# Optimization experiments

Hardware: AMD Instinct MI355X
Metric: run time of the kernel (lower is better)

The kernel has to match this reference:

```python
import jax, jax.numpy as jnp
import numpy as np

D_MODEL = 1024
N_HEADS = 16
D_HEAD = D_MODEL // N_HEADS
B, T = 2, 2048


def setup_inputs() -> dict:
    key = jax.random.key(0)
    ks = jax.random.split(key, 8)
    s = 1.0 / np.sqrt(D_MODEL)
    return {
        "x": jax.random.normal(ks[0], (B, T, D_MODEL), dtype=jnp.float32),
        "ln_g": jnp.ones((D_MODEL,), jnp.float32),
        "ln_b": jnp.zeros((D_MODEL,), jnp.float32),
        "w_qkv": jax.random.normal(ks[1], (D_MODEL, 3 * D_MODEL), jnp.float32) * s,
        "b_qkv": jnp.zeros((3 * D_MODEL,), jnp.float32),
        "w_gate": jax.random.normal(ks[2], (D_MODEL, D_MODEL), jnp.float32) * s,
        "b_gate": jnp.zeros((D_MODEL,), jnp.float32),
        "w_proj": jax.random.normal(ks[3], (D_MODEL, D_MODEL), jnp.float32) * s,
        "b_proj": jnp.zeros((D_MODEL,), jnp.float32),
    }


def reference(x, ln_g, ln_b, w_qkv, b_qkv, w_gate, b_gate, w_proj, b_proj):
    Bb, Tt, Dd = x.shape
    H, dh = N_HEADS, D_HEAD

    # LayerNorm (eps=1e-5, torch default)
    mu = jnp.mean(x, axis=-1, keepdims=True)
    var = jnp.mean((x - mu) ** 2, axis=-1, keepdims=True)
    x_norm = (x - mu) / jnp.sqrt(var + 1e-5) * ln_g + ln_b

    qkv = x_norm @ w_qkv + b_qkv
    q, k, v = jnp.split(qkv, 3, axis=-1)

    # concept gate on the RAW input x (not x_norm), normalized by its mean
    gate_sig = jax.nn.sigmoid(x @ w_gate + b_gate)
    gate_norm = gate_sig / (jnp.mean(gate_sig, axis=-1, keepdims=True) + 1e-5)
    q = q * gate_norm
    k = k * gate_norm

    # [B,T,D] -> [B,H,T,dh]
    def to_heads(t):
        return t.reshape(Bb, Tt, H, dh).transpose(0, 2, 1, 3)

    q, k, v = to_heads(q), to_heads(k), to_heads(v)

    q = jax.nn.elu(q) + 1.0
    k = jax.nn.elu(k) + 1.0

    # materialized outer-product cumsum (faithful to source formulation)
    kv = jnp.einsum("bhtd,bhtm->bhtdm", k, v)          # [B,H,T,dh,dh]
    kv_cumsum = jnp.cumsum(kv, axis=2)
    out_num = jnp.einsum("bhtd,bhtdm->bhtm", q, kv_cumsum)
    k_cumsum = jnp.cumsum(k, axis=2)
    out_den = jnp.einsum("bhtd,bhtd->bht", q, k_cumsum)[..., None] + 1e-5
    out = out_num / out_den                              # [B,H,T,dh]

    out = out.transpose(0, 2, 1, 3).reshape(Bb, Tt, Dd)
    return out @ w_proj + b_proj
```

## Files before the change

kernel.cpp:

```cpp
#include <hip/hip_runtime.h>
#include <math.h>

constexpr int D      = 1024;
constexpr int H      = 16;
constexpr int DH     = 64;
constexpr int Bb     = 2;
constexpr int T      = 2048;
constexpr int BT     = Bb * T;
constexpr int CHUNK  = 64;
constexpr int NC     = T / CHUNK;
constexpr int LS     = 72;

typedef __attribute__((ext_vector_type(8))) short bf16x8;
typedef __attribute__((ext_vector_type(4))) float f32x4;

#define GLOAD_LDS16(gp, lp) \
    __builtin_amdgcn_global_load_lds((const __attribute__((address_space(1))) void*)(gp), \
                                     (__attribute__((address_space(3))) void*)(lp), 16, 0, 0)

__device__ __forceinline__ short to_bf16(float f) {
    unsigned u = __float_as_uint(f);
    unsigned r = (u + 0x7fffu + ((u >> 16) & 1u)) >> 16;
    return (short)r;
}
__device__ __forceinline__ float bf2f(short s) {
    return __uint_as_float(((unsigned)(unsigned short)s) << 16);
}

__device__ __forceinline__ float block_sum_256(float v, float* sbuf) {
    #pragma unroll
    for (int off = 32; off > 0; off >>= 1) v += __shfl_down(v, off, 64);
    int lane = threadIdx.x & 63;
    int wid  = threadIdx.x >> 6;
    if (lane == 0) sbuf[wid] = v;
    __syncthreads();
    float r = (threadIdx.x < 4) ? sbuf[threadIdx.x] : 0.0f;
    r += __shfl_down(r, 2, 64);
    r += __shfl_down(r, 1, 64);
    if (threadIdx.x == 0) sbuf[0] = r;
    __syncthreads();
    float outv = sbuf[0];
    __syncthreads();
    return outv;
}

__device__ __forceinline__ float elu1(float x) {
    return x > 0.0f ? x + 1.0f : expf(x);
}

__global__ __launch_bounds__(256) void ln_kernel(const float* __restrict__ x,
                                                 const float* __restrict__ g,
                                                 const float* __restrict__ b,
                                                 short* __restrict__ ynb,
                                                 short* __restrict__ xb) {
    __shared__ float sbuf[4];
    int row = blockIdx.x;
    const float* xr = x + (size_t)row * D;
    int c = threadIdx.x * 4;
    float4 xv = *(const float4*)(xr + c);
    float mu = block_sum_256(xv.x + xv.y + xv.z + xv.w, sbuf) * (1.0f / D);
    float d0 = xv.x - mu, d1 = xv.y - mu, d2 = xv.z - mu, d3 = xv.w - mu;
    float var = block_sum_256(d0*d0 + d1*d1 + d2*d2 + d3*d3, sbuf) * (1.0f / D);
    float rstd = rsqrtf(var + 1e-5f);
    float4 gv = *(const float4*)(g + c);
    float4 bv = *(const float4*)(b + c);
    short4 o, xo;
    o.x = to_bf16(d0 * rstd * gv.x + bv.x);
    o.y = to_bf16(d1 * rstd * gv.y + bv.y);
    o.z = to_bf16(d2 * rstd * gv.z + bv.z);
    o.w = to_bf16(d3 * rstd * gv.w + bv.w);
    xo.x = to_bf16(xv.x); xo.y = to_bf16(xv.y);
    xo.z = to_bf16(xv.z); xo.w = to_bf16(xv.w);
    *(short4*)(ynb + (size_t)row * D + c) = o;
    *(short4*)(xb  + (size_t)row * D + c) = xo;
}

__global__ __launch_bounds__(256) void transpose_all_kernel(const float* __restrict__ wq,
                                                            const float* __restrict__ wg,
                                                            const float* __restrict__ wp,
                                                            short* __restrict__ wTcomb,
                                                            short* __restrict__ wTp) {
    __shared__ short tile[32][33];
    int bid = blockIdx.x;
    const float* W; short* Wt; int N; int t;
    if (bid < 3072)      { W = wq; Wt = wTcomb;                        N = 3072; t = bid; }
    else if (bid < 4096) { W = wg; Wt = wTcomb + (size_t)3072 * 1024;  N = 1024; t = bid - 3072; }
    else                 { W = wp; Wt = wTp;                           N = 1024; t = bid - 4096; }
    int ntiles = N >> 5;
    int nb = (t % ntiles) * 32, kb = (t / ntiles) * 32;
    int tx = threadIdx.x & 31, ty = threadIdx.x >> 5;
    #pragma unroll
    for (int i = 0; i < 4; ++i) {
        int k = kb + ty + i * 8;
        tile[ty + i * 8][tx] = to_bf16(W[(size_t)k * N + nb + tx]);
    }
    __syncthreads();
    #pragma unroll
    for (int i = 0; i < 4; ++i) {
        int n = nb + ty + i * 8;
        Wt[(size_t)n * 1024 + kb + tx] = tile[tx][ty + i * 8];
    }
}

__global__ __launch_bounds__(256) void gemm_fused_qkvgate(const short* __restrict__ xnb,
                                                          const short* __restrict__ xb,
                                                          const short* __restrict__ Wt,
                                                          const float* __restrict__ b_qkv,
                                                          const float* __restrict__ b_gate,
                                                          short* __restrict__ qkvb,
                                                          short* __restrict__ gateb) {
    constexpr int BK = 32, K = 1024;
    __shared__ short Als[128 * BK];
    __shared__ short Bls[128 * BK];

    const int tid  = threadIdx.x;
    const int wave = tid >> 6;
    const int lane = tid & 63;
    const int row0 = blockIdx.y * 128;
    const int col0 = blockIdx.x * 128;
    const bool isg = (col0 >= 3 * D);
    const short* A = isg ? xb : xnb;
    const int wm = (wave & 1) * 64;
    const int wn = (wave >> 1) * 64;

    f32x4 acc[4][4] = {};
    const int srow = lane >> 2;
    const int skk  = (lane & 3) * 8;
    const int fr = lane & 15;
    const int fk = (lane >> 4) * 8;

    for (int k0 = 0; k0 < K; k0 += BK) {
        __syncthreads();
        #pragma unroll
        for (int u = 0; u < 2; ++u) {
            int cchunk = wave * 2 + u;
            int r = cchunk * 16 + srow;
            GLOAD_LDS16(A  + (size_t)(row0 + r) * K + k0 + skk, &Als[cchunk * 512]);
            GLOAD_LDS16(Wt + (size_t)(col0 + r) * K + k0 + skk, &Bls[cchunk * 512]);
        }
        __syncthreads();

        bf16x8 af[4], bfr[4];
        #pragma unroll
        for (int i = 0; i < 4; ++i) {
            af[i]  = *(const bf16x8*)&Als[(wm + i * 16 + fr) * BK + fk];
            bfr[i] = *(const bf16x8*)&Bls[(wn + i * 16 + fr) * BK + fk];
        }
        #pragma unroll
        for (int mi = 0; mi < 4; ++mi)
            #pragma unroll
            for (int ni = 0; ni < 4; ++ni)
                acc[mi][ni] = __builtin_amdgcn_mfma_f32_16x16x32_bf16(af[mi], bfr[ni], acc[mi][ni], 0, 0, 0);
    }

    const int ccol  = lane & 15;
    const int crow4 = (lane >> 4) * 4;
    const float* biasp = isg ? (b_gate - 3 * D) : b_qkv;
    short* dst  = isg ? gateb : qkvb;
    const int stride = isg ? D : 3 * D;
    const int csub   = isg ? 3 * D : 0;
    #pragma unroll
    for (int mi = 0; mi < 4; ++mi) {
        #pragma unroll
        for (int ni = 0; ni < 4; ++ni) {
            int col = col0 + wn + ni * 16 + ccol;
            float bv = biasp[col];
            #pragma unroll
            for (int r = 0; r < 4; ++r) {
                int row = row0 + wm + mi * 16 + crow4 + r;
                dst[(size_t)row * stride + (col - csub)] = to_bf16(acc[mi][ni][r] + bv);
            }
        }
    }
}

__global__ __launch_bounds__(256) void gate_apply_inplace(short* __restrict__ qkvb,
                                                          const short* __restrict__ gateb) {
    __shared__ float sbuf[4];
    int row = blockIdx.x;
    int c = threadIdx.x * 4;
    short4 gl = *(const short4*)(gateb + (size_t)row * D + c);
    float s0 = 1.0f / (1.0f + expf(-bf2f(gl.x)));
    float s1 = 1.0f / (1.0f + expf(-bf2f(gl.y)));
    float s2 = 1.0f / (1.0f + expf(-bf2f(gl.z)));
    float s3 = 1.0f / (1.0f + expf(-bf2f(gl.w)));
    float mean = block_sum_256(s0 + s1 + s2 + s3, sbuf) * (1.0f / D);
    float inv = 1.0f / (mean + 1e-5f);
    float g0 = s0 * inv, g1 = s1 * inv, g2 = s2 * inv, g3 = s3 * inv;

    short* qp = qkvb + (size_t)row * (3 * D) + c;
    short* kp = qp + D;
    short4 qv = *(short4*)qp;
    short4 kv = *(short4*)kp;
    qv.x = to_bf16(elu1(bf2f(qv.x) * g0)); qv.y = to_bf16(elu1(bf2f(qv.y) * g1));
    qv.z = to_bf16(elu1(bf2f(qv.z) * g2)); qv.w = to_bf16(elu1(bf2f(qv.w) * g3));
    kv.x = to_bf16(elu1(bf2f(kv.x) * g0)); kv.y = to_bf16(elu1(bf2f(kv.y) * g1));
    kv.z = to_bf16(elu1(bf2f(kv.z) * g2)); kv.w = to_bf16(elu1(bf2f(kv.w) * g3));
    *(short4*)qp = qv;
    *(short4*)kp = kv;
}

__global__ __launch_bounds__(256) void chunk_state_mfma(const short* __restrict__ qkvb,
                                                        float* __restrict__ SxT,
                                                        float* __restrict__ zbuf) {
    __shared__ short Kt[DH * LS];
    __shared__ short Vt[DH * LS];
    int idx = blockIdx.x;
    int c = idx & (NC - 1), h = (idx >> 5) & (H - 1), b = idx >> 9;
    size_t bt0 = (size_t)b * T + c * CHUNK;
    const short* kbase = qkvb + bt0 * (3 * D) + D + h * DH;
    const short* vbase = qkvb + bt0 * (3 * D) + 2 * D + h * DH;
    int tid = threadIdx.x;

    #pragma unroll
    for (int l = 0; l < 2; ++l) {
        int i  = tid + l * 256;
        int t  = i >> 3;
        int d8 = (i & 7) * 8;
        bf16x8 kv = *(const bf16x8*)(kbase + (size_t)t * (3 * D) + d8);
        bf16x8 vv = *(const bf16x8*)(vbase + (size_t)t * (3 * D) + d8);
        #pragma unroll
        for (int j = 0; j < 8; ++j) {
            Kt[(d8 + j) * LS + t] = kv[j];
            Vt[(d8 + j) * LS + t] = vv[j];
        }
    }
    __syncthreads();

    const int wv = tid >> 6, lane = tid & 63;
    const int fr = lane & 15, quad = lane >> 4;
    const int fk = quad * 8, crow4 = quad * 4, ccol = lane & 15;
    const int mbase = wv * 16;

    bf16x8 af[2];
    af[0] = *(const bf16x8*)&Vt[(mbase + fr) * LS + fk];
    af[1] = *(const bf16x8*)&Vt[(mbase + fr) * LS + 32 + fk];

    f32x4 acc[4] = {};
    #pragma unroll
    for (int n = 0; n < 4; ++n) {
        #pragma unroll
        for (int ck = 0; ck < 2; ++ck) {
            bf16x8 bk = *(const bf16x8*)&Kt[(n * 16 + fr) * LS + ck * 32 + fk];
            acc[n] = __builtin_amdgcn_mfma_f32_16x16x32_bf16(af[ck], bk, acc[n], 0, 0, 0);
        }
    }

    float* Sd = SxT + (size_t)idx * (DH * DH);
    #pragma unroll
    for (int n = 0; n < 4; ++n)
        #pragma unroll
        for (int r = 0; r < 4; ++r)
            Sd[(mbase + crow4 + r) * DH + n * 16 + ccol] = acc[n][r];

    if (tid < DH) {
        float zs = 0.0f;
        for (int t = 0; t < CHUNK; ++t) zs += bf2f(Kt[tid * LS + t]);
        zbuf[(size_t)idx * DH + tid] = zs;
    }
}

__global__ __launch_bounds__(256) void chunk_prefix_kernel(const float* __restrict__ S,
                                                           short* __restrict__ Spb,
                                                           float* __restrict__ z) {
    int bh   = blockIdx.x >> 4;
    int part = blockIdx.x & 15;
    int e    = part * 256 + threadIdx.x;
    const float* Sb = S + (size_t)bh * NC * DH * DH;
    short* Pb = Spb + (size_t)bh * NC * DH * DH;
    float acc = 0.0f;
    for (int c = 0; c < NC; ++c) {
        size_t off = (size_t)c * DH * DH + e;
        float t = Sb[off];
        Pb[off] = to_bf16(acc);
        acc += t;
    }
    if (part == 0 && threadIdx.x < DH) {
        float* zb = z + (size_t)bh * NC * DH;
        float za = 0.0f;
        for (int c = 0; c < NC; ++c) {
            float* p = zb + c * DH + threadIdx.x;
            float t = *p; *p = za; za += t;
        }
    }
}

__global__ __launch_bounds__(256) void chunk_attn_mfma(const short* __restrict__ qkvb,
                                                       const short* __restrict__ Spb,
                                                       const float* __restrict__ zbuf,
                                                       short* __restrict__ attnb) {
    __shared__ short Qs[CHUNK * LS];
    __shared__ short Ks[CHUNK * LS];
    __shared__ short Vt[DH * LS];
    __shared__ short Ss[DH * LS];
    __shared__ short As[CHUNK * LS];
    __shared__ float zpL[DH];
    __shared__ float den[CHUNK];

    int idx = blockIdx.x;
    int c = idx & (NC - 1), h = (idx >> 5) & (H - 1), b = idx >> 9;
    size_t bt0 = (size_t)b * T + c * CHUNK;
    const short* qbase = qkvb + bt0 * (3 * D) + h * DH;
    const short* kbase = qbase + D;
    const short* vbase = qbase + 2 * D;
    const short* spb = Spb + (size_t)idx * (DH * DH);
    int tid = threadIdx.x;

    #pragma unroll
    for (int l = 0; l < 2; ++l) {
        int i  = tid + l * 256;
        int t  = i >> 3;
        int d8 = (i & 7) * 8;
        *(bf16x8*)&Qs[t * LS + d8] = *(const bf16x8*)(qbase + (size_t)t * (3 * D) + d8);
        *(bf16x8*)&Ks[t * LS + d8] = *(const bf16x8*)(kbase + (size_t)t * (3 * D) + d8);
        bf16x8 vv = *(const bf16x8*)(vbase + (size_t)t * (3 * D) + d8);
        #pragma unroll
        for (int j = 0; j < 8; ++j) Vt[(d8 + j) * LS + t] = vv[j];
        *(bf16x8*)&Ss[t * LS + d8] = *(const bf16x8*)(spb + (size_t)i * 8);
    }
    if (tid < DH) zpL[tid] = zbuf[(size_t)idx * DH + tid];
    __syncthreads();

    const int wv = tid >> 6, lane = tid & 63;
    const int fr = lane & 15, quad = lane >> 4;
    const int fk = quad * 8, crow4 = quad * 4, ccol = lane & 15;
    const int tbase = wv * 16;

    bf16x8 aq[2];
    aq[0] = *(const bf16x8*)&Qs[(tbase + fr) * LS + fk];
    aq[1] = *(const bf16x8*)&Qs[(tbase + fr) * LS + 32 + fk];

    f32x4 accs[4] = {};
    #pragma unroll
    for (int n = 0; n < 4; ++n) {
        #pragma unroll
        for (int ck = 0; ck < 2; ++ck) {
            bf16x8 bk = *(const bf16x8*)&Ks[(n * 16 + fr) * LS + ck * 32 + fk];
            accs[n] = __builtin_amdgcn_mfma_f32_16x16x32_bf16(aq[ck], bk, accs[n], 0, 0, 0);
        }
    }

    float part[4] = {0.f, 0.f, 0.f, 0.f};
    #pragma unroll
    for (int n = 0; n < 4; ++n) {
        #pragma unroll
        for (int r = 0; r < 4; ++r) {
            int tt = tbase + crow4 + r;
            int ss = n * 16 + ccol;
            float v = (ss <= tt) ? accs[n][r] : 0.0f;
            part[r] += v;
            As[tt * LS + ss] = to_bf16(v);
        }
    }
    #pragma unroll
    for (int r = 0; r < 4; ++r) {
        part[r] += __shfl_xor(part[r], 1, 64);
        part[r] += __shfl_xor(part[r], 2, 64);
        part[r] += __shfl_xor(part[r], 4, 64);
        part[r] += __shfl_xor(part[r], 8, 64);
    }
    if (fr == 0) {
        #pragma unroll
        for (int r = 0; r < 4; ++r) den[tbase + crow4 + r] = part[r];
    }
    __syncthreads();

    if (tid < CHUNK) {
        float qz = 0.0f;
        #pragma unroll 8
        for (int d = 0; d < DH; ++d) qz += bf2f(Qs[tid * LS + d]) * zpL[d];
        den[tid] += qz + 1e-5f;
    }

    f32x4 acco[4] = {};
    #pragma unroll
    for (int m4 = 0; m4 < 4; ++m4) {
        #pragma unroll
        for (int ck = 0; ck < 2; ++ck) {
            bf16x8 bs = *(const bf16x8*)&Ss[(m4 * 16 + fr) * LS + ck * 32 + fk];
            acco[m4] = __builtin_amdgcn_mfma_f32_16x16x32_bf16(aq[ck], bs, acco[m4], 0, 0, 0);
        }
    }
    bf16x8 aa[2];
    aa[0] = *(const bf16x8*)&As[(tbase + fr) * LS + fk];
    aa[1] = *(const bf16x8*)&As[(tbase + fr) * LS + 32 + fk];
    #pragma unroll
    for (int m4 = 0; m4 < 4; ++m4) {
        #pragma unroll
        for (int ck = 0; ck < 2; ++ck) {
            bf16x8 bv = *(const bf16x8*)&Vt[(m4 * 16 + fr) * LS + ck * 32 + fk];
            acco[m4] = __builtin_amdgcn_mfma_f32_16x16x32_bf16(aa[ck], bv, acco[m4], 0, 0, 0);
        }
    }
    __syncthreads();

    short* obase = attnb + bt0 * D + h * DH;
    #pragma unroll
    for (int r = 0; r < 4; ++r) {
        int tt = tbase + crow4 + r;
        float rv = 1.0f / den[tt];
        #pragma unroll
        for (int m4 = 0; m4 < 4; ++m4)
            obase[(size_t)tt * D + m4 * 16 + ccol] = to_bf16(acco[m4][r] * rv);
    }
}

__global__ __launch_bounds__(256) void gemm_proj64(const short* __restrict__ A,
                                                   const short* __restrict__ Bt,
                                                   const float* __restrict__ bias,
                                                   float* __restrict__ C) {
    constexpr int BK = 32, K = 1024, N = 1024;
    __shared__ short Als[64 * BK];
    __shared__ short Bls[128 * BK];

    const int tid  = threadIdx.x;
    const int wave = tid >> 6;
    const int lane = tid & 63;
    const int row0 = blockIdx.y * 64;
    const int col0 = blockIdx.x * 128;
    const int wn = wave * 32;

    f32x4 acc[4][2] = {};
    const int srow = lane >> 2;
    const int skk  = (lane & 3) * 8;
    const int fr = lane & 15;
    const int fk = (lane >> 4) * 8;

    for (int k0 = 0; k0 < K; k0 += BK) {
        __syncthreads();
        #pragma unroll
        for (int u = 0; u < 3; ++u) {
            int cc = wave * 3 + u;
            if (cc < 4) {
                int r = cc * 16 + srow;
                GLOAD_LDS16(A + (size_t)(row0 + r) * K + k0 + skk, &Als[cc * 512]);
            } else {
                int c2 = cc - 4;
                int r = c2 * 16 + srow;
                GLOAD_LDS16(Bt + (size_t)(col0 + r) * K + k0 + skk, &Bls[c2 * 512]);
            }
        }
        __syncthreads();

        bf16x8 af[4], bfr[2];
        #pragma unroll
        for (int i = 0; i < 4; ++i) af[i] = *(const bf16x8*)&Als[(i * 16 + fr) * BK + fk];
        #pragma unroll
        for (int j = 0; j < 2; ++j) bfr[j] = *(const bf16x8*)&Bls[(wn + j * 16 + fr) * BK + fk];
        #pragma unroll
        for (int mi = 0; mi < 4; ++mi)
            #pragma unroll
            for (int ni = 0; ni < 2; ++ni)
                acc[mi][ni] = __builtin_amdgcn_mfma_f32_16x16x32_bf16(af[mi], bfr[ni], acc[mi][ni], 0, 0, 0);
    }

    const int ccol  = lane & 15;
    const int crow4 = (lane >> 4) * 4;
    #pragma unroll
    for (int mi = 0; mi < 4; ++mi) {
        #pragma unroll
        for (int ni = 0; ni < 2; ++ni) {
            int col = col0 + wn + ni * 16 + ccol;
            float bv = bias[col];
            #pragma unroll
            for (int r = 0; r < 4; ++r) {
                int row = row0 + mi * 16 + crow4 + r;
                C[(size_t)row * N + col] = acc[mi][ni][r] + bv;
            }
        }
    }
}

extern "C" void kernel_launch(void* const* d_in, const int* in_sizes, int n_in,
                              void* d_out, int out_size, void* d_ws, size_t ws_size,
                              hipStream_t stream) {
    const float* x      = (const float*)d_in[0];
    const float* ln_g   = (const float*)d_in[1];
    const float* ln_b   = (const float*)d_in[2];
    const float* w_qkv  = (const float*)d_in[3];
    const float* b_qkv  = (const float*)d_in[4];
    const float* w_gate = (const float*)d_in[5];
    const float* b_gate = (const float*)d_in[6];
    const float* w_proj = (const float*)d_in[7];
    const float* b_proj = (const float*)d_in[8];
    float* out = (float*)d_out;

    short* xnb   = (short*)d_ws;
    short* xb    = xnb + (size_t)BT * D;
    short* wTc   = xb + (size_t)BT * D;
    short* wTp   = wTc + (size_t)4096 * 1024;
    short* qkvb  = wTp + (size_t)D * D;
    short* gateb = qkvb + (size_t)BT * 3 * D;
    short* attnb = gateb + (size_t)BT * D;
    float* zbuf  = (float*)(attnb + (size_t)BT * D);
    float* SxT   = (float*)xnb;
    short* Spb   = wTc;

    ln_kernel<<<BT, 256, 0, stream>>>(x, ln_g, ln_b, xnb, xb);
    transpose_all_kernel<<<5120, 256, 0, stream>>>(w_qkv, w_gate, w_proj, wTc, wTp);
    gemm_fused_qkvgate<<<dim3(32, 32), 256, 0, stream>>>(
        xnb, xb, wTc, b_qkv, b_gate, qkvb, gateb);
    gate_apply_inplace<<<BT, 256, 0, stream>>>(qkvb, gateb);
    chunk_state_mfma<<<Bb * H * NC, 256, 0, stream>>>(qkvb, SxT, zbuf);
    chunk_prefix_kernel<<<Bb * H * 16, 256, 0, stream>>>(SxT, Spb, zbuf);
    chunk_attn_mfma<<<Bb * H * NC, 256, 0, stream>>>(qkvb, Spb, zbuf, attnb);
    gemm_proj64<<<dim3(D / 128, BT / 64), 256, 0, stream>>>(attnb, wTp, b_proj, out);
}
```

Before: 209.9 us.

## Fuse gating into GEMM epilogue and attention loads, merge prep kernels, swizzle LDS

```diff
diff --git a/kernel.cpp b/kernel.cpp
--- a/kernel.cpp
+++ b/kernel.cpp
@@ -45,60 +45,64 @@
 }
 
 __device__ __forceinline__ float elu1(float x) {
-    return x > 0.0f ? x + 1.0f : expf(x);
-}
-
-__global__ __launch_bounds__(256) void ln_kernel(const float* __restrict__ x,
-                                                 const float* __restrict__ g,
-                                                 const float* __restrict__ b,
-                                                 short* __restrict__ ynb,
-                                                 short* __restrict__ xb) {
+    return x > 0.0f ? x + 1.0f : __expf(x);
+}
+
+__global__ __launch_bounds__(256) void pre_kernel(const float* __restrict__ x,
+                                                  const float* __restrict__ g,
+                                                  const float* __restrict__ b,
+                                                  const float* __restrict__ wq,
+                                                  const float* __restrict__ wg,
+                                                  const float* __restrict__ wp,
+                                                  short* __restrict__ ynb,
+                                                  short* __restrict__ xbb,
+                                                  short* __restrict__ wTcomb,
+                                                  short* __restrict__ wTp,
+                                                  float* __restrict__ gmean) {
     __shared__ float sbuf[4];
-    int row = blockIdx.x;
-    const float* xr = x + (size_t)row * D;
-    int c = threadIdx.x * 4;
-    float4 xv = *(const float4*)(xr + c);
-    float mu = block_sum_256(xv.x + xv.y + xv.z + xv.w, sbuf) * (1.0f / D);
-    float d0 = xv.x - mu, d1 = xv.y - mu, d2 = xv.z - mu, d3 = xv.w - mu;
-    float var = block_sum_256(d0*d0 + d1*d1 + d2*d2 + d3*d3, sbuf) * (1.0f / D);
-    float rstd = rsqrtf(var + 1e-5f);
-    float4 gv = *(const float4*)(g + c);
-    float4 bv = *(const float4*)(b + c);
-    short4 o, xo;
-    o.x = to_bf16(d0 * rstd * gv.x + bv.x);
-    o.y = to_bf16(d1 * rstd * gv.y + bv.y);
-    o.z = to_bf16(d2 * rstd * gv.z + bv.z);
-    o.w = to_bf16(d3 * rstd * gv.w + bv.w);
-    xo.x = to_bf16(xv.x); xo.y = to_bf16(xv.y);
-    xo.z = to_bf16(xv.z); xo.w = to_bf16(xv.w);
-    *(short4*)(ynb + (size_t)row * D + c) = o;
-    *(short4*)(xb  + (size_t)row * D + c) = xo;
-}
-
-__global__ __launch_bounds__(256) void transpose_all_kernel(const float* __restrict__ wq,
-                                                            const float* __restrict__ wg,
-                                                            const float* __restrict__ wp,
-                                                            short* __restrict__ wTcomb,
-                                                            short* __restrict__ wTp) {
     __shared__ short tile[32][33];
     int bid = blockIdx.x;
-    const float* W; short* Wt; int N; int t;
-    if (bid < 3072)      { W = wq; Wt = wTcomb;                        N = 3072; t = bid; }
-    else if (bid < 4096) { W = wg; Wt = wTcomb + (size_t)3072 * 1024;  N = 1024; t = bid - 3072; }
-    else                 { W = wp; Wt = wTp;                           N = 1024; t = bid - 4096; }
-    int ntiles = N >> 5;
-    int nb = (t % ntiles) * 32, kb = (t / ntiles) * 32;
-    int tx = threadIdx.x & 31, ty = threadIdx.x >> 5;
-    #pragma unroll
-    for (int i = 0; i < 4; ++i) {
-        int k = kb + ty + i * 8;
-        tile[ty + i * 8][tx] = to_bf16(W[(size_t)k * N + nb + tx]);
-    }
-    __syncthreads();
-    #pragma unroll
-    for (int i = 0; i < 4; ++i) {
-        int n = nb + ty + i * 8;
-        Wt[(size_t)n * 1024 + kb + tx] = tile[tx][ty + i * 8];
+    if (bid < BT) {
+        int row = bid;
+        if (threadIdx.x == 0) gmean[row] = 0.0f;
+        const float* xr = x + (size_t)row * D;
+        int c = threadIdx.x * 4;
+        float4 xv = *(const float4*)(xr + c);
+        float mu = block_sum_256(xv.x + xv.y + xv.z + xv.w, sbuf) * (1.0f / D);
+        float d0 = xv.x - mu, d1 = xv.y - mu, d2 = xv.z - mu, d3 = xv.w - mu;
+        float var = block_sum_256(d0*d0 + d1*d1 + d2*d2 + d3*d3, sbuf) * (1.0f / D);
+        float rstd = rsqrtf(var + 1e-5f);
+        float4 gv = *(const float4*)(g + c);
+        float4 bv = *(const float4*)(b + c);
+        short4 o, xo;
+        o.x = to_bf16(d0 * rstd * gv.x + bv.x);
+        o.y = to_bf16(d1 * rstd * gv.y + bv.y);
+        o.z = to_bf16(d2 * rstd * gv.z + bv.z);
+        o.w = to_bf16(d3 * rstd * gv.w + bv.w);
+        xo.x = to_bf16(xv.x); xo.y = to_bf16(xv.y);
+        xo.z = to_bf16(xv.z); xo.w = to_bf16(xv.w);
+        *(short4*)(ynb + (size_t)row * D + c) = o;
+        *(short4*)(xbb + (size_t)row * D + c) = xo;
+    } else {
+        int t2 = bid - BT;
+        const float* W; short* Wt; int N; int t;
+        if (t2 < 3072)      { W = wq; Wt = wTcomb;                       N = 3072; t = t2; }
+        else if (t2 < 4096) { W = wg; Wt = wTcomb + (size_t)3072 * 1024; N = 1024; t = t2 - 3072; }
+        else                { W = wp; Wt = wTp;                          N = 1024; t = t2 - 4096; }
+        int ntiles = N >> 5;
+        int nb = (t % ntiles) * 32, kb = (t / ntiles) * 32;
+        int tx = threadIdx.x & 31, ty = threadIdx.x >> 5;
+        #pragma unroll
+        for (int i = 0; i < 4; ++i) {
+            int k = kb + ty + i * 8;
+            tile[ty + i * 8][tx] = to_bf16(W[(size_t)k * N + nb + tx]);
+        }
+        __syncthreads();
+        #pragma unroll
+        for (int i = 0; i < 4; ++i) {
+            int n = nb + ty + i * 8;
+            Wt[(size_t)n * 1024 + kb + tx] = tile[tx][ty + i * 8];
+        }
     }
 }
 
@@ -108,10 +112,12 @@
                                                           const float* __restrict__ b_qkv,
                                                           const float* __restrict__ b_gate,
                                                           short* __restrict__ qkvb,
-                                                          short* __restrict__ gateb) {
+                                                          short* __restrict__ sigb,
+                                                          float* __restrict__ gmean) {
     constexpr int BK = 32, K = 1024;
     __shared__ short Als[128 * BK];
     __shared__ short Bls[128 * BK];
+    __shared__ float gsum[128];
 
     const int tid  = threadIdx.x;
     const int wave = tid >> 6;
@@ -123,11 +129,13 @@
     const int wm = (wave & 1) * 64;
     const int wn = (wave >> 1) * 64;
 
+    if (isg && tid < 128) gsum[tid] = 0.0f;
+
     f32x4 acc[4][4] = {};
     const int srow = lane >> 2;
-    const int skk  = (lane & 3) * 8;
-    const int fr = lane & 15;
-    const int fk = (lane >> 4) * 8;
+    const int skk  = (((lane & 3) ^ ((lane >> 3) & 3)) * 8);
+    const int fr   = lane & 15;
+    const int fks  = (((lane >> 4) ^ ((lane >> 1) & 3)) * 8);
 
     for (int k0 = 0; k0 < K; k0 += BK) {
         __syncthreads();
@@ -143,8 +151,8 @@
         bf16x8 af[4], bfr[4];
         #pragma unroll
         for (int i = 0; i < 4; ++i) {
-            af[i]  = *(const bf16x8*)&Als[(wm + i * 16 + fr) * BK + fk];
-            bfr[i] = *(const bf16x8*)&Bls[(wn + i * 16 + fr) * BK + fk];
+            af[i]  = *(const bf16x8*)&Als[(wm + i * 16 + fr) * BK + fks];
+            bfr[i] = *(const bf16x8*)&Bls[(wn + i * 16 + fr) * BK + fks];
         }
         #pragma unroll
         for (int mi = 0; mi < 4; ++mi)
@@ -155,61 +163,56 @@
 
     const int ccol  = lane & 15;
     const int crow4 = (lane >> 4) * 4;
-    const float* biasp = isg ? (b_gate - 3 * D) : b_qkv;
-    short* dst  = isg ? gateb : qkvb;
-    const int stride = isg ? D : 3 * D;
-    const int csub   = isg ? 3 * D : 0;
-    #pragma unroll
-    for (int mi = 0; mi < 4; ++mi) {
-        #pragma unroll
-        for (int ni = 0; ni < 4; ++ni) {
-            int col = col0 + wn + ni * 16 + ccol;
-            float bv = biasp[col];
+    if (!isg) {
+        #pragma unroll
+        for (int mi = 0; mi < 4; ++mi) {
+            #pragma unroll
+            for (int ni = 0; ni < 4; ++ni) {
+                int col = col0 + wn + ni * 16 + ccol;
+                float bv = b_qkv[col];
+                #pragma unroll
+                for (int r = 0; r < 4; ++r) {
+                    int row = row0 + wm + mi * 16 + crow4 + r;
+                    qkvb[(size_t)row * (3 * D) + col] = to_bf16(acc[mi][ni][r] + bv);
+                }
+            }
+        }
+    } else {
+        #pragma unroll
+        for (int mi = 0; mi < 4; ++mi) {
             #pragma unroll
             for (int r = 0; r < 4; ++r) {
-                int row = row0 + wm + mi * 16 + crow4 + r;
-                dst[(size_t)row * stride + (col - csub)] = to_bf16(acc[mi][ni][r] + bv);
+                int lrow = wm + mi * 16 + crow4 + r;
+                float psum = 0.0f;
+                #pragma unroll
+                for (int ni = 0; ni < 4; ++ni) {
+                    int col = col0 + wn + ni * 16 + ccol - 3 * D;
+                    float v = acc[mi][ni][r] + b_gate[col];
+                    float sv = 1.0f / (1.0f + __expf(-v));
+                    sigb[(size_t)(row0 + lrow) * D + col] = to_bf16(sv);
+                    psum += sv;
+                }
+                atomicAdd(&gsum[lrow], psum);
             }
         }
-    }
-}
-
-__global__ __launch_bounds__(256) void gate_apply_inplace(short* __restrict__ qkvb,
-                                                          const short* __restrict__ gateb) {
-    __shared__ float sbuf[4];
-    int row = blockIdx.x;
-    int c = threadIdx.x * 4;
-    short4 gl = *(const short4*)(gateb + (size_t)row * D + c);
-    float s0 = 1.0f / (1.0f + expf(-bf2f(gl.x)));
-    float s1 = 1.0f / (1.0f + expf(-bf2f(gl.y)));
-    float s2 = 1.0f / (1.0f + expf(-bf2f(gl.z)));
-    float s3 = 1.0f / (1.0f + expf(-bf2f(gl.w)));
-    float mean = block_sum_256(s0 + s1 + s2 + s3, sbuf) * (1.0f / D);
-    float inv = 1.0f / (mean + 1e-5f);
-    float g0 = s0 * inv, g1 = s1 * inv, g2 = s2 * inv, g3 = s3 * inv;
-
-    short* qp = qkvb + (size_t)row * (3 * D) + c;
-    short* kp = qp + D;
-    short4 qv = *(short4*)qp;
-    short4 kv = *(short4*)kp;
-    qv.x = to_bf16(elu1(bf2f(qv.x) * g0)); qv.y = to_bf16(elu1(bf2f(qv.y) * g1));
-    qv.z = to_bf16(elu1(bf2f(qv.z) * g2)); qv.w = to_bf16(elu1(bf2f(qv.w) * g3));
-    kv.x = to_bf16(elu1(bf2f(kv.x) * g0)); kv.y = to_bf16(elu1(bf2f(kv.y) * g1));
-    kv.z = to_bf16(elu1(bf2f(kv.z) * g2)); kv.w = to_bf16(elu1(bf2f(kv.w) * g3));
-    *(short4*)qp = qv;
-    *(short4*)kp = kv;
+        __syncthreads();
+        if (tid < 128) atomicAdd(&gmean[row0 + tid], gsum[tid]);
+    }
 }
 
 __global__ __launch_bounds__(256) void chunk_state_mfma(const short* __restrict__ qkvb,
-                                                        float* __restrict__ SxT,
-                                                        float* __restrict__ zbuf) {
+                                                        const short* __restrict__ sigb,
+                                                        const float* __restrict__ gmean,
+                                                        float* __restrict__ Sc,
+                                                        float* __restrict__ zc) {
     __shared__ short Kt[DH * LS];
     __shared__ short Vt[DH * LS];
     int idx = blockIdx.x;
     int c = idx & (NC - 1), h = (idx >> 5) & (H - 1), b = idx >> 9;
     size_t bt0 = (size_t)b * T + c * CHUNK;
     const short* kbase = qkvb + bt0 * (3 * D) + D + h * DH;
-    const short* vbase = qkvb + bt0 * (3 * D) + 2 * D + h * DH;
+    const short* vbase = kbase + D;
+    const short* sbase = sigb + bt0 * D + h * DH;
     int tid = threadIdx.x;
 
     #pragma unroll
@@ -217,11 +220,14 @@
         int i  = tid + l * 256;
         int t  = i >> 3;
         int d8 = (i & 7) * 8;
+        float invm = 1.0f / (gmean[bt0 + t] * (1.0f / D) + 1e-5f);
         bf16x8 kv = *(const bf16x8*)(kbase + (size_t)t * (3 * D) + d8);
         bf16x8 vv = *(const bf16x8*)(vbase + (size_t)t * (3 * D) + d8);
+        bf16x8 sg = *(const bf16x8*)(sbase + (size_t)t * D + d8);
         #pragma unroll
         for (int j = 0; j < 8; ++j) {
-            Kt[(d8 + j) * LS + t] = kv[j];
+            float gn = bf2f(sg[j]) * invm;
+            Kt[(d8 + j) * LS + t] = to_bf16(elu1(bf2f(kv[j]) * gn));
             Vt[(d8 + j) * LS + t] = vv[j];
         }
     }
@@ -246,7 +252,7 @@
         }
     }
 
-    float* Sd = SxT + (size_t)idx * (DH * DH);
+    float* Sd = Sc + (size_t)idx * (DH * DH);
     #pragma unroll
     for (int n = 0; n < 4; ++n)
         #pragma unroll
@@ -256,7 +262,7 @@
     if (tid < DH) {
         float zs = 0.0f;
         for (int t = 0; t < CHUNK; ++t) zs += bf2f(Kt[tid * LS + t]);
-        zbuf[(size_t)idx * DH + tid] = zs;
+        zc[(size_t)idx * DH + tid] = zs;
     }
 }
 
@@ -286,8 +292,10 @@
 }
 
 __global__ __launch_bounds__(256) void chunk_attn_mfma(const short* __restrict__ qkvb,
+                                                       const short* __restrict__ sigb,
+                                                       const float* __restrict__ gmean,
                                                        const short* __restrict__ Spb,
-                                                       const float* __restrict__ zbuf,
+                                                       const float* __restrict__ zc,
                                                        short* __restrict__ attnb) {
     __shared__ short Qs[CHUNK * LS];
     __shared__ short Ks[CHUNK * LS];
@@ -303,6 +311,7 @@
     const short* qbase = qkvb + bt0 * (3 * D) + h * DH;
     const short* kbase = qbase + D;
     const short* vbase = qbase + 2 * D;
+    const short* sbase = sigb + bt0 * D + h * DH;
     const short* spb = Spb + (size_t)idx * (DH * DH);
     int tid = threadIdx.x;
 
@@ -311,14 +320,24 @@
         int i  = tid + l * 256;
         int t  = i >> 3;
         int d8 = (i & 7) * 8;
-        *(bf16x8*)&Qs[t * LS + d8] = *(const bf16x8*)(qbase + (size_t)t * (3 * D) + d8);
-        *(bf16x8*)&Ks[t * LS + d8] = *(const bf16x8*)(kbase + (size_t)t * (3 * D) + d8);
+        float invm = 1.0f / (gmean[bt0 + t] * (1.0f / D) + 1e-5f);
+        bf16x8 qv = *(const bf16x8*)(qbase + (size_t)t * (3 * D) + d8);
+        bf16x8 kv = *(const bf16x8*)(kbase + (size_t)t * (3 * D) + d8);
         bf16x8 vv = *(const bf16x8*)(vbase + (size_t)t * (3 * D) + d8);
-        #pragma unroll
-        for (int j = 0; j < 8; ++j) Vt[(d8 + j) * LS + t] = vv[j];
+        bf16x8 sg = *(const bf16x8*)(sbase + (size_t)t * D + d8);
+        bf16x8 qg, kg;
+        #pragma unroll
+        for (int j = 0; j < 8; ++j) {
+            float gn = bf2f(sg[j]) * invm;
+            qg[j] = to_bf16(elu1(bf2f(qv[j]) * gn));
+            kg[j] = to_bf16(elu1(bf2f(kv[j]) * gn));
+            Vt[(d8 + j) * LS + t] = vv[j];
+        }
+        *(bf16x8*)&Qs[t * LS + d8] = qg;
+        *(bf16x8*)&Ks[t * LS + d8] = kg;
         *(bf16x8*)&Ss[t * LS + d8] = *(const bf16x8*)(spb + (size_t)i * 8);
     }
-    if (tid < DH) zpL[tid] = zbuf[(size_t)idx * DH + tid];
+    if (tid < DH) zpL[tid] = zc[(size_t)idx * DH + tid];
     __syncthreads();
 
     const int wv = tid >> 6, lane = tid & 63;
@@ -422,9 +441,9 @@
 
     f32x4 acc[4][2] = {};
     const int srow = lane >> 2;
-    const int skk  = (lane & 3) * 8;
-    const int fr = lane & 15;
-    const int fk = (lane >> 4) * 8;
+    const int skk  = (((lane & 3) ^ ((lane >> 3) & 3)) * 8);
+    const int fr   = lane & 15;
+    const int fks  = (((lane >> 4) ^ ((lane >> 1) & 3)) * 8);
 
     for (int k0 = 0; k0 < K; k0 += BK) {
         __syncthreads();
@@ -444,9 +463,11 @@
 
         bf16x8 af[4], bfr[2];
         #pragma unroll
-        for (int i = 0; i < 4; ++i) af[i] = *(const bf16x8*)&Als[(i * 16 + fr) * BK + fk];
-        #pragma unroll
-        for (int j = 0; j < 2; ++j) bfr[j] = *(const bf16x8*)&Bls[(wn + j * 16 + fr) * BK + fk];
+        for (int i = 0; i < 4; ++i)
+            af[i] = *(const bf16x8*)&Als[(i * 16 + fr) * BK + fks];
+        #pragma unroll
+        for (int j = 0; j < 2; ++j)
+            bfr[j] = *(const bf16x8*)&Bls[(wn + j * 16 + fr) * BK + fks];
         #pragma unroll
         for (int mi = 0; mi < 4; ++mi)
             #pragma unroll
@@ -490,19 +511,19 @@
     short* wTc   = xb + (size_t)BT * D;
     short* wTp   = wTc + (size_t)4096 * 1024;
     short* qkvb  = wTp + (size_t)D * D;
-    short* gateb = qkvb + (size_t)BT * 3 * D;
-    short* attnb = gateb + (size_t)BT * D;
-    float* zbuf  = (float*)(attnb + (size_t)BT * D);
-    float* SxT   = (float*)xnb;
+    short* sigb  = qkvb + (size_t)BT * 3 * D;
+    short* attnb = sigb + (size_t)BT * D;
+    float* zc    = (float*)(attnb + (size_t)BT * D);
+    float* gmean = zc + (size_t)Bb * H * NC * DH;
+    float* Sc    = (float*)xnb;
     short* Spb   = wTc;
 
-    ln_kernel<<<BT, 256, 0, stream>>>(x, ln_g, ln_b, xnb, xb);
-    transpose_all_kernel<<<5120, 256, 0, stream>>>(w_qkv, w_gate, w_proj, wTc, wTp);
+    pre_kernel<<<BT + 5120, 256, 0, stream>>>(x, ln_g, ln_b, w_qkv, w_gate, w_proj,
+                                              xnb, xb, wTc, wTp, gmean);
     gemm_fused_qkvgate<<<dim3(32, 32), 256, 0, stream>>>(
-        xnb, xb, wTc, b_qkv, b_gate, qkvb, gateb);
-    gate_apply_inplace<<<BT, 256, 0, stream>>>(qkvb, gateb);
-    chunk_state_mfma<<<Bb * H * NC, 256, 0, stream>>>(qkvb, SxT, zbuf);
-    chunk_prefix_kernel<<<Bb * H * 16, 256, 0, stream>>>(SxT, Spb, zbuf);
-    chunk_attn_mfma<<<Bb * H * NC, 256, 0, stream>>>(qkvb, Spb, zbuf, attnb);
+        xnb, xb, wTc, b_qkv, b_gate, qkvb, sigb, gmean);
+    chunk_state_mfma<<<Bb * H * NC, 256, 0, stream>>>(qkvb, sigb, gmean, Sc, zc);
+    chunk_prefix_kernel<<<Bb * H * 16, 256, 0, stream>>>(Sc, Spb, zc);
+    chunk_attn_mfma<<<Bb * H * NC, 256, 0, stream>>>(qkvb, sigb, gmean, Spb, zc, attnb);
     gemm_proj64<<<dim3(D / 128, BT / 64), 256, 0, stream>>>(attnb, wTp, b_proj, out);
 }
```

Measured after the change: 223.0 us. +6.2%, slower.
